# Kernel optimization log

Hardware: AMD Instinct MI355X
Metric: run time of the kernel (lower is better)

The kernel has to match this reference:

```python
import jax, jax.numpy as jnp
import numpy as np

M, K, N = 64, 4096, 14336


def setup_inputs() -> dict:
    key = jax.random.key(0)
    k1, k2, k3, k4, k5 = jax.random.split(key, 5)
    x = jax.random.normal(k1, (M, K), dtype=jnp.float32)
    # int8-valued weights stored as int32 (values in [-128, 128))
    weight = jax.random.randint(k2, (K, N), -128, 128, dtype=jnp.int32)
    # per-channel dequant params (one per output channel N)
    antiquant_scale = jax.random.uniform(k3, (N,), dtype=jnp.float32, minval=0.001, maxval=0.02)
    antiquant_offset = jax.random.normal(k4, (N,), dtype=jnp.float32)
    bias = jax.random.normal(k5, (N,), dtype=jnp.float32)
    return {"x": x, "weight": weight, "antiquant_scale": antiquant_scale,
            "antiquant_offset": antiquant_offset, "bias": bias}


def reference(x, weight, antiquant_scale, antiquant_offset, bias):
    # npu_weight_quant_batchmatmul, per-channel antiquant, no output quant:
    # out = x @ ((weight + antiquant_offset) * antiquant_scale) + bias
    w_deq = (weight.astype(x.dtype) + antiquant_offset[None, :]) * antiquant_scale[None, :]  # [K, N]
    out = jnp.einsum('mk,kn->mn', x, w_deq) + bias[None, :]  # [M, N]
    return out
```

## Files before the change

### kernel.cpp

```cpp
#include <hip/hip_runtime.h>
#include <hip/hip_bf16.h>

#define M_DIM 64
#define K_DIM 4096
#define N_DIM 14336
#define NBLKS 224
#define KW 1024
#define WCHUNKS 32

typedef __attribute__((ext_vector_type(8))) short bf16x8;
typedef __attribute__((ext_vector_type(4))) float f32x4;
typedef unsigned short u16;

__global__ void prep_split(const float* __restrict__ x, u16* __restrict__ xh,
                           u16* __restrict__ xl) {
  int tg = blockIdx.x * blockDim.x + threadIdx.x;
  int kb = tg & 511;
  int m = tg >> 9;
  const float* xp = x + m * K_DIM + kb * 8;
  u16 hs[8], ls[8];
#pragma unroll
  for (int j = 0; j < 8; ++j) {
    float v = xp[j];
    unsigned hv = __float_as_uint(v) & 0xFFFF0000u;
    float r = v - __uint_as_float(hv);
    hs[j] = (u16)(hv >> 16);
    ls[j] = (u16)(__float_as_uint(r) >> 16);
  }
  int o = kb * (M_DIM * 8) + m * 8;
  *(uint4*)(xh + o) = *(uint4*)hs;
  *(uint4*)(xl + o) = *(uint4*)ls;
}

__global__ void rowsum_k(const float* __restrict__ x, float* __restrict__ rs) {
  int m = blockIdx.x;
  int t = threadIdx.x;
  float s = 0.f;
  for (int k = t; k < K_DIM; k += 256) s += x[m * K_DIM + k];
#pragma unroll
  for (int off = 32; off > 0; off >>= 1) s += __shfl_down(s, off, 64);
  __shared__ float red[4];
  if ((t & 63) == 0) red[t >> 6] = s;
  __syncthreads();
  if (t == 0) rs[m] = red[0] + red[1] + red[2] + red[3];
}

__global__ __launch_bounds__(256, 1) void wqmm(
    const int* __restrict__ W, const u16* __restrict__ xh,
    const u16* __restrict__ xl, const float* __restrict__ rowsum,
    const float* __restrict__ scale, const float* __restrict__ offset,
    const float* __restrict__ bias, float* __restrict__ out) {
  __shared__ __align__(16) float red[4][64][66];

  const int t = threadIdx.x;
  const int lane = t & 63;
  const int wv = t >> 6;
  const int quad = lane >> 4;
  const int lnk = lane & 15;
  const int nbase = blockIdx.x * 64;
  const int k0 = wv * KW;

  int laneoff[4];
#pragma unroll
  for (int f = 0; f < 4; ++f)
    laneoff[f] = quad * 8 * N_DIM + nbase + lnk + f * 16;

  const u16* xhp = xh + (size_t)(wv * 128 + quad) * 512 + lnk * 8;
  const u16* xlp = xl + (size_t)(wv * 128 + quad) * 512 + lnk * 8;

  f32x4 acc[4][4] = {};
  int raw[2][4][8];
  bf16x8 abh[2][4], abl[2][4];

#define LOADW(CC, BUF)                                            \
  do {                                                            \
    _Pragma("unroll") for (int j = 0; j < 8; ++j) {               \
      const int* bj = W + (size_t)(k0 + (CC) * 32 + j) * N_DIM;   \
      _Pragma("unroll") for (int f = 0; f < 4; ++f)               \
          raw[BUF][f][j] = bj[laneoff[f]];                        \
    }                                                             \
  } while (0)

#define LOADA(CC, BUF)                                            \
  do {                                                            \
    const u16* ahc = xhp + (CC) * 2048;                           \
    const u16* alc = xlp + (CC) * 2048;                           \
    _Pragma("unroll") for (int mt = 0; mt < 4; ++mt) {            \
      abh[BUF][mt] = *(const bf16x8*)(ahc + mt * 128);            \
      abl[BUF][mt] = *(const bf16x8*)(alc + mt * 128);            \
    }                                                             \
  } while (0)

#define COMPUTE(CC, BUF)                                                     \
  do {                                                                       \
    bf16x8 bfr[4];                                                           \
    _Pragma("unroll") for (int f = 0; f < 4; ++f) {                          \
      union {                                                                \
        int i4[4];                                                           \
        bf16x8 v;                                                            \
      } u;                                                                   \
      _Pragma("unroll") for (int wd = 0; wd < 4; ++wd) {                     \
        unsigned lo = __float_as_uint((float)raw[BUF][f][2 * wd]);           \
        unsigned hi = __float_as_uint((float)raw[BUF][f][2 * wd + 1]);       \
        u.i4[wd] = (int)((lo >> 16) | (hi & 0xFFFF0000u));        \
      }                                                                      \
      bfr[f] = u.v;                                                          \
    }                                                                        \
    _Pragma("unroll") for (int mt = 0; mt < 4; ++mt) {                       \
      _Pragma("unroll") for (int f = 0; f < 4; ++f) {                        \
        acc[mt][f] = __builtin_amdgcn_mfma_f32_16x16x32_bf16(                \
            abh[BUF][mt], bfr[f], acc[mt][f], 0, 0, 0);                      \
        acc[mt][f] = __builtin_amdgcn_mfma_f32_16x16x32_bf16(                \
            abl[BUF][mt], bfr[f], acc[mt][f], 0, 0, 0);                      \
      }                                                                      \
    }                                                                        \
  } while (0)

  LOADW(0, 0);
  LOADA(0, 0);
  for (int c = 0; c < WCHUNKS; c += 2) {
    LOADW(c + 1, 1);
    LOADA(c + 1, 1);
    COMPUTE(c, 0);
    if (c + 2 < WCHUNKS) {
      LOADW(c + 2, 0);
      LOADA(c + 2, 0);
    }
    COMPUTE(c + 1, 1);
  }
#undef LOADW
#undef LOADA
#undef COMPUTE

#pragma unroll
  for (int f = 0; f < 4; ++f)
#pragma unroll
    for (int mt = 0; mt < 4; ++mt)
#pragma unroll
      for (int r = 0; r < 4; ++r)
        red[wv][mt * 16 + quad * 4 + r][f * 16 + lnk] = acc[mt][f][r];
  __syncthreads();

#pragma unroll
  for (int i = 0; i < 16; ++i) {
    int idx = t + i * 256;
    int m = idx >> 6;
    int nc = idx & 63;
    float s = red[0][m][nc] + red[1][m][nc] + red[2][m][nc] + red[3][m][nc];
    int n = nbase + nc;
    float sc = scale[n];
    out[(size_t)m * N_DIM + n] = s * sc + sc * offset[n] * rowsum[m] + bias[n];
  }
}

extern "C" void kernel_launch(void* const* d_in, const int* in_sizes, int n_in,
                              void* d_out, int out_size, void* d_ws,
                              size_t ws_size, hipStream_t stream) {
  const float* x = (const float*)d_in[0];
  const int* W = (const int*)d_in[1];
  const float* scale = (const float*)d_in[2];
  const float* offset = (const float*)d_in[3];
  const float* bias = (const float*)d_in[4];
  float* out = (float*)d_out;

  char* wsb = (char*)d_ws;
  u16* xh = (u16*)wsb;
  u16* xl = xh + (size_t)M_DIM * K_DIM;
  float* rowsum = (float*)(xl + (size_t)M_DIM * K_DIM);

  prep_split<<<128, 256, 0, stream>>>(x, xh, xl);
  rowsum_k<<<64, 256, 0, stream>>>(x, rowsum);
  wqmm<<<NBLKS, 256, 0, stream>>>(W, xh, xl, rowsum, scale, offset, bias, out);
}
```

Measured before the change: 342.8 us.

## Split K across eight waves per block and fuse rowsum into prep kernel

The matmul kernel now runs 512 threads per block, with eight waves each covering 512 of K instead of four waves covering 1024. This doubles the number of weight loads in flight to hide HBM latency on the weight stream. The partial sums of the extra waves are added into shared memory in a two-phase reduction. The separate rowsum kernel is folded into the split kernel, removing one launch, and the bf16 packing now uses a single byte-permute instruction. The risks are more register pressure under the new launch bounds and an extra barrier in the reduction.

```diff
diff --git a/kernel.cpp b/kernel.cpp
--- a/kernel.cpp
+++ b/kernel.cpp
@@ -5,47 +5,47 @@
 #define K_DIM 4096
 #define N_DIM 14336
 #define NBLKS 224
-#define KW 1024
-#define WCHUNKS 32
+#define KW 512
+#define WCHUNKS 16
 
 typedef __attribute__((ext_vector_type(8))) short bf16x8;
 typedef __attribute__((ext_vector_type(4))) float f32x4;
 typedef unsigned short u16;
 
-__global__ void prep_split(const float* __restrict__ x, u16* __restrict__ xh,
-                           u16* __restrict__ xl) {
-  int tg = blockIdx.x * blockDim.x + threadIdx.x;
-  int kb = tg & 511;
-  int m = tg >> 9;
-  const float* xp = x + m * K_DIM + kb * 8;
+__global__ __launch_bounds__(512) void prep_split(
+    const float* __restrict__ x, u16* __restrict__ xh, u16* __restrict__ xl,
+    float* __restrict__ rs) {
+  const int m = blockIdx.x;
+  const int t = threadIdx.x;
+  const float* xp = x + m * K_DIM + t * 8;
   u16 hs[8], ls[8];
+  float s = 0.f;
 #pragma unroll
   for (int j = 0; j < 8; ++j) {
     float v = xp[j];
+    s += v;
     unsigned hv = __float_as_uint(v) & 0xFFFF0000u;
     float r = v - __uint_as_float(hv);
     hs[j] = (u16)(hv >> 16);
     ls[j] = (u16)(__float_as_uint(r) >> 16);
   }
-  int o = kb * (M_DIM * 8) + m * 8;
+  int o = t * (M_DIM * 8) + m * 8;
   *(uint4*)(xh + o) = *(uint4*)hs;
   *(uint4*)(xl + o) = *(uint4*)ls;
+#pragma unroll
+  for (int off = 32; off > 0; off >>= 1) s += __shfl_down(s, off, 64);
+  __shared__ float red[8];
+  if ((t & 63) == 0) red[t >> 6] = s;
+  __syncthreads();
+  if (t == 0) {
+    float a = 0.f;
+#pragma unroll
+    for (int i = 0; i < 8; ++i) a += red[i];
+    rs[m] = a;
+  }
 }
 
-__global__ void rowsum_k(const float* __restrict__ x, float* __restrict__ rs) {
-  int m = blockIdx.x;
-  int t = threadIdx.x;
-  float s = 0.f;
-  for (int k = t; k < K_DIM; k += 256) s += x[m * K_DIM + k];
-#pragma unroll
-  for (int off = 32; off > 0; off >>= 1) s += __shfl_down(s, off, 64);
-  __shared__ float red[4];
-  if ((t & 63) == 0) red[t >> 6] = s;
-  __syncthreads();
-  if (t == 0) rs[m] = red[0] + red[1] + red[2] + red[3];
-}
-
-__global__ __launch_bounds__(256, 1) void wqmm(
+__global__ __launch_bounds__(512, 2) void wqmm(
     const int* __restrict__ W, const u16* __restrict__ xh,
     const u16* __restrict__ xl, const float* __restrict__ rowsum,
     const float* __restrict__ scale, const float* __restrict__ offset,
@@ -65,8 +65,8 @@
   for (int f = 0; f < 4; ++f)
     laneoff[f] = quad * 8 * N_DIM + nbase + lnk + f * 16;
 
-  const u16* xhp = xh + (size_t)(wv * 128 + quad) * 512 + lnk * 8;
-  const u16* xlp = xl + (size_t)(wv * 128 + quad) * 512 + lnk * 8;
+  const u16* xhp = xh + (size_t)(wv * 64 + quad) * 512 + lnk * 8;
+  const u16* xlp = xl + (size_t)(wv * 64 + quad) * 512 + lnk * 8;
 
   f32x4 acc[4][4] = {};
   int raw[2][4][8];
@@ -102,7 +102,8 @@
       _Pragma("unroll") for (int wd = 0; wd < 4; ++wd) {                     \
         unsigned lo = __float_as_uint((float)raw[BUF][f][2 * wd]);           \
         unsigned hi = __float_as_uint((float)raw[BUF][f][2 * wd + 1]);       \
-        u.i4[wd] = (int)((lo >> 16) | (hi & 0xFFFF0000u));        \
+               \
+        u.i4[wd] = (int)__builtin_amdgcn_perm(hi, lo, 0x07060302u);          \
       }                                                                      \
       bfr[f] = u.v;                                                          \
     }                                                                        \
@@ -132,18 +133,30 @@
 #undef LOADA
 #undef COMPUTE
 
+  if (wv < 4) {
 #pragma unroll
-  for (int f = 0; f < 4; ++f)
+    for (int f = 0; f < 4; ++f)
 #pragma unroll
-    for (int mt = 0; mt < 4; ++mt)
+      for (int mt = 0; mt < 4; ++mt)
 #pragma unroll
-      for (int r = 0; r < 4; ++r)
-        red[wv][mt * 16 + quad * 4 + r][f * 16 + lnk] = acc[mt][f][r];
+        for (int r = 0; r < 4; ++r)
+          red[wv][mt * 16 + quad * 4 + r][f * 16 + lnk] = acc[mt][f][r];
+  }
+  __syncthreads();
+  if (wv >= 4) {
+#pragma unroll
+    for (int f = 0; f < 4; ++f)
+#pragma unroll
+      for (int mt = 0; mt < 4; ++mt)
+#pragma unroll
+        for (int r = 0; r < 4; ++r)
+          red[wv - 4][mt * 16 + quad * 4 + r][f * 16 + lnk] += acc[mt][f][r];
+  }
   __syncthreads();
 
 #pragma unroll
-  for (int i = 0; i < 16; ++i) {
-    int idx = t + i * 256;
+  for (int i = 0; i < 8; ++i) {
+    int idx = t + i * 512;
     int m = idx >> 6;
     int nc = idx & 63;
     float s = red[0][m][nc] + red[1][m][nc] + red[2][m][nc] + red[3][m][nc];
@@ -168,7 +181,6 @@
   u16* xl = xh + (size_t)M_DIM * K_DIM;
   float* rowsum = (float*)(xl + (size_t)M_DIM * K_DIM);
 
-  prep_split<<<128, 256, 0, stream>>>(x, xh, xl);
-  rowsum_k<<<64, 256, 0, stream>>>(x, rowsum);
-  wqmm<<<NBLKS, 256, 0, stream>>>(W, xh, xl, rowsum, scale, offset, bias, out);
+  prep_split<<<64, 512, 0, stream>>>(x, xh, xl, rowsum);
+  wqmm<<<NBLKS, 512, 0, stream>>>(W, xh, xl, rowsum, scale, offset, bias, out);
 }
```

Result: faster. 333.7 us (-2.6%).
